# Kernel tuning notes

Measured on AMD Instinct MI355X. Metric: run time of the kernel, lower is better.

## Reference

```python
import jax, jax.numpy as jnp
import numpy as np

B, S, H = 8, 32, 2048          # batch, block (query) length, hidden size
NH, NKV, HD = 16, 2, 128       # attention heads, kv heads, head_dim
KV_LEN = 8192                  # block kv-cache length
GROUPS = NH // NKV
SCALE = HD ** -0.5


def rotate_half(x):
    x1, x2 = jnp.split(x, 2, axis=-1)
    return jnp.concatenate((-x2, x1), axis=-1)


def setup_inputs() -> dict:
    key = jax.random.key(0)
    ks = jax.random.split(key, 12)
    inv_freq = 1.0 / (10000.0 ** (jnp.arange(0, HD, 2, dtype=jnp.float32) / HD))
    pos = jnp.arange(S, dtype=jnp.float32)[:, None] * inv_freq[None, :]  # [S, HD/2]
    ang = jnp.concatenate([pos, pos], axis=-1)                           # [S, HD]
    cos = jnp.broadcast_to(jnp.cos(ang)[None], (B, S, HD))
    sin = jnp.broadcast_to(jnp.sin(ang)[None], (B, S, HD))
    s = 0.02
    return {
        'hidden_states': jax.random.normal(ks[0], (B, S, H), jnp.float32),
        'cos': cos,
        'sin': sin,
        'k_cache': jax.random.normal(ks[1], (B, NKV, KV_LEN, HD), jnp.float32),
        'v_cache': jax.random.normal(ks[2], (B, NKV, KV_LEN, HD), jnp.float32),
        'attention_mask': jnp.zeros((B, 1, S, KV_LEN), jnp.float32),
        'replace_position': 4096,
        'q_w': jax.random.normal(ks[3], (H, NH * HD), jnp.float32) * s,
        'q_b': jax.random.normal(ks[4], (NH * HD,), jnp.float32) * s,
        'k_w': jax.random.normal(ks[5], (H, NKV * HD), jnp.float32) * s,
        'k_b': jax.random.normal(ks[6], (NKV * HD,), jnp.float32) * s,
        'v_w': jax.random.normal(ks[7], (H, NKV * HD), jnp.float32) * s,
        'v_b': jax.random.normal(ks[8], (NKV * HD,), jnp.float32) * s,
        'o_w': jax.random.normal(ks[9], (NH * HD, H), jnp.float32) * s,
    }


def reference(hidden_states, cos, sin, k_cache, v_cache, attention_mask,
              replace_position, q_w, q_b, k_w, k_b, v_w, v_b, o_w):
    # fused QKV projections -> [B, heads, S, HD]
    q = (hidden_states @ q_w + q_b).reshape(B, S, NH, HD).transpose(0, 2, 1, 3)
    k = (hidden_states @ k_w + k_b).reshape(B, S, NKV, HD).transpose(0, 2, 1, 3)
    v = (hidden_states @ v_w + v_b).reshape(B, S, NKV, HD).transpose(0, 2, 1, 3)

    # RoPE (cos/sin unsqueezed on the head dim)
    c = cos[:, None]  # [B,1,S,HD]
    s_ = sin[:, None]
    q = q * c + rotate_half(q) * s_
    k = k * c + rotate_half(k) * s_

    # block KV-cache in-place update at replace_position
    k_all = jax.lax.dynamic_update_slice(k_cache, k, (0, 0, replace_position, 0))
    v_all = jax.lax.dynamic_update_slice(v_cache, v, (0, 0, replace_position, 0))

    # GQA: expand kv heads to match attention heads
    k_all = jnp.repeat(k_all, GROUPS, axis=1)  # [B,NH,KV,HD]
    v_all = jnp.repeat(v_all, GROUPS, axis=1)

    # SDPA with additive mask (is_causal=False)
    scores = jnp.einsum('bhqd,bhkd->bhqk', q, k_all) * SCALE + attention_mask
    probs = jax.nn.softmax(scores, axis=-1)
    attn = jnp.einsum('bhqk,bhkd->bhqd', probs, v_all)  # [B,NH,S,HD]

    out = attn.transpose(0, 2, 1, 3).reshape(B, S, NH * HD)
    return out @ o_w
```

## Files before the change

### kernel.cpp

```cpp
#include <hip/hip_runtime.h>
#include <hip/hip_bf16.h>

#define B_    8
#define S_    32
#define H_    2048
#define NH_   16
#define NKV_  2
#define HD_   128
#define KV_   8192
#define G_    8
#define M_    256
#define NQKV  2560
#define NSP   16
#define KT_   64
#define NT_   8
#define SCALE_ 0.08838834764831845f
#define CFIX_  8.0f

typedef __bf16 bf16x8 __attribute__((ext_vector_type(8)));
typedef float  f32x4  __attribute__((ext_vector_type(4)));
typedef float  f32x16 __attribute__((ext_vector_type(16)));

__device__ __forceinline__ unsigned short f2b(float f){
  unsigned u = __float_as_uint(f);
  u = u + 0x7FFFu + ((u>>16)&1u);
  return (unsigned short)(u>>16);
}
__device__ __forceinline__ float b2f(unsigned short h){
  return __uint_as_float(((unsigned)h)<<16);
}
__device__ __forceinline__ unsigned pk2(float a, float b){
  return (unsigned)f2b(a) | ((unsigned)f2b(b)<<16);
}
__device__ __forceinline__ unsigned cvtpk(float lo, float hi){
  unsigned r;
  asm("v_cvt_pk_bf16_f32 %0, %1, %2" : "=v"(r) : "v"(lo), "v"(hi));
  return r;
}
__device__ __forceinline__ bf16x8 ld_frag(const unsigned short* p){
  union { uint4 u; bf16x8 b; } cv;
  cv.u = *(const uint4*)p;
  return cv.b;
}
__device__ __forceinline__ f32x4 mf(bf16x8 a, bf16x8 b, f32x4 c){
  return __builtin_amdgcn_mfma_f32_16x16x32_bf16(a, b, c, 0, 0, 0);
}
__device__ __forceinline__ f32x16 mf32(bf16x8 a, bf16x8 b, f32x16 c){
  return __builtin_amdgcn_mfma_f32_32x32x16_bf16(a, b, c, 0, 0, 0);
}
__device__ __forceinline__ int swiK(int row, int col){
  return row*128 + (col ^ ((((row)&15) ^ ((row>>1)&8)) << 3));
}
__device__ __forceinline__ int swiV(int row, int col){
  return row*64 + (col ^ (((row)&7) << 3));
}

__global__ __launch_bounds__(256) void k_cvt(const float* __restrict__ x,
                                             unsigned short* __restrict__ y){
  const int i = (blockIdx.x*256 + threadIdx.x)*4;
  const float4 v = *(const float4*)(x + i);
  ushort4 o; o.x=f2b(v.x); o.y=f2b(v.y); o.z=f2b(v.z); o.w=f2b(v.w);
  *(ushort4*)(y + i) = o;
}

__global__ __launch_bounds__(256) void k_gemm_qkv(
    const unsigned short* __restrict__ A,
    const float* __restrict__ qw, const float* __restrict__ kw, const float* __restrict__ vw,
    const float* __restrict__ qbv, const float* __restrict__ kbv, const float* __restrict__ vbv,
    float* __restrict__ rawp)
{
  __shared__ unsigned short As[64][56];
  __shared__ unsigned short Bs[64][56];
  const int n0 = blockIdx.x*64, m0 = blockIdx.y*64, kz = blockIdx.z;
  const float* W; const float* bias; int ldw, wc0;
  if(n0 < 2048)      { W=qw; bias=qbv; ldw=2048; wc0=n0; }
  else if(n0 < 2304) { W=kw; bias=kbv; ldw=256;  wc0=n0-2048; }
  else               { W=vw; bias=vbv; ldw=256;  wc0=n0-2304; }
  const int t = threadIdx.x, lane = t&63, wid = t>>6;
  const int wr = wid>>1, wc = wid&1, l15 = lane&15, lq = lane>>4;
  const int ar = t>>2,  ac = (t&3)*8;
  const int bk = t>>5,  bn = (t&31)*2;
  f32x4 acc[2][2] = {};
  for(int k0 = kz*1024; k0 < kz*1024 + 1024; k0 += 32){
    __syncthreads();
    *(uint4*)(&As[ar][ac]) = *(const uint4*)(A + (m0+ar)*2048 + k0 + ac);
    #pragma unroll
    for(int p=0;p<4;p++){
      const int kk = bk + p*8;
      const float2 wv = *(const float2*)(W + (long)(k0+kk)*ldw + wc0 + bn);
      Bs[bn  ][kk] = f2b(wv.x);
      Bs[bn+1][kk] = f2b(wv.y);
    }
    __syncthreads();
    const bf16x8 a0 = ld_frag(&As[wr*32      + l15][lq*8]);
    const bf16x8 a1 = ld_frag(&As[wr*32 + 16 + l15][lq*8]);
    const bf16x8 b0 = ld_frag(&Bs[wc*32      + l15][lq*8]);
    const bf16x8 b1 = ld_frag(&Bs[wc*32 + 16 + l15][lq*8]);
    acc[0][0] = mf(a0,b0,acc[0][0]);
    acc[0][1] = mf(a0,b1,acc[0][1]);
    acc[1][0] = mf(a1,b0,acc[1][0]);
    acc[1][1] = mf(a1,b1,acc[1][1]);
  }
  float* out = rawp + (long)kz*M_*NQKV;
  #pragma unroll
  for(int mi=0;mi<2;mi++)
    #pragma unroll
    for(int nj=0;nj<2;nj++){
      const int col = n0 + wc*32 + nj*16 + l15;
      const float bv = kz ? 0.f : bias[wc0 + wc*32 + nj*16 + l15];
      #pragma unroll
      for(int rr=0;rr<4;rr++){
        const int row = m0 + wr*32 + mi*16 + lq*4 + rr;
        out[row*NQKV + col] = acc[mi][nj][rr] + bv;
      }
    }
}

__global__ __launch_bounds__(128) void k_rope(
    const float* __restrict__ rawp, const float* __restrict__ cosb, const float* __restrict__ sinb,
    unsigned short* __restrict__ Qb, float* __restrict__ KnF, float* __restrict__ VnF)
{
  const int r = blockIdx.x, hh = blockIdx.y, d = threadIdx.x;
  const int b = r>>5, s = r&31;
  const float cv = cosb[(b*S_+s)*HD_ + d];
  const float sv = sinb[(b*S_+s)*HD_ + d];
  const int dp = (d<64)? d+64 : d-64;
  #define RAW2(c) (rawp[r*NQKV + (c)] + rawp[(long)M_*NQKV + r*NQKV + (c)])
  if(hh < 16){
    const float x  = RAW2(hh*HD_ + d);
    const float xo = RAW2(hh*HD_ + dp);
    const float y  = x*cv + ((d<64)? -xo : xo)*sv;
    const int kvh = hh>>3, g = hh&7;
    Qb[((long)(b*NKV_+kvh)*M_ + g*S_ + s)*HD_ + d] = f2b(y);
  } else if(hh < 18){
    const int kvh = hh-16;
    const float x  = RAW2(2048 + kvh*HD_ + d);
    const float xo = RAW2(2048 + kvh*HD_ + dp);
    KnF[((long)(b*NKV_+kvh)*S_ + s)*HD_ + d] = x*cv + ((d<64)? -xo : xo)*sv;
  } else {
    const int kvh = hh-18;
    VnF[((long)(b*NKV_+kvh)*S_ + s)*HD_ + d] = RAW2(2304 + kvh*HD_ + d);
  }
  #undef RAW2
}

__global__ __launch_bounds__(256) void k_mswz(const float* __restrict__ mask,
                                              float* __restrict__ msw){
  const int g = blockIdx.x*256 + threadIdx.x;
  const int b = g >> 16, q = (g>>11)&31, c4 = g & 2047;
  const int kv = c4*4;
  const int sp = kv>>9, tt = (kv>>6)&7, kvt = (kv>>5)&1, r4 = (kv>>3)&3, hi = (kv>>2)&1;
  const int lane = q + 32*hi;
  float4 v = *(const float4*)(mask + ((long)b*S_ + q)*KV_ + kv);
  v.x -= CFIX_; v.y -= CFIX_; v.z -= CFIX_; v.w -= CFIX_;
  const long dst = ((((long)(b*NSP+sp)*NT_ + tt)*64 + lane)*8 + kvt*4 + r4);
  *(float4*)(msw + dst*4) = v;
}

__global__ __launch_bounds__(512, 2) void k_attn(
    const unsigned short* __restrict__ Qb,
    const float* __restrict__ KnF, const float* __restrict__ VnF,
    const float* __restrict__ kc, const float* __restrict__ vc,
    const float* __restrict__ msw, const int* __restrict__ rpp,
    unsigned short* __restrict__ num, float* __restrict__ mbuf, float* __restrict__ lbuf)
{
  __shared__ __align__(16) unsigned short lds[2][2][KT_*128];
  const int sp = blockIdx.x, kvh = blockIdx.y, b = blockIdx.z;
  const int bk = b*NKV_ + kvh;
  const int rp = *rpp;
  const int t = threadIdx.x, lane = t&63, wid = t>>6;
  const int l31 = lane&31, hi = lane>>5;
  const int kvbase = sp*(KV_/NSP);
  const int krow = t>>3, kc0 = (t&7)*16;
  const int vhd  = t&127, vkq = t>>7;
  const int cbsK = (hi*8) ^ ((((l31)&15) ^ ((l31>>1)&8)) << 3);
  const int cbsV = (hi*8) ^ (((l31)&7) << 3);
  const int rowK = l31*128, rowV = l31*64;
  const int wk0 = swiK(krow, kc0), wk1 = swiK(krow, kc0+8);
  const int wv0 = swiV(vhd, vkq*16), wv1 = swiV(vhd, vkq*16+8);

  bf16x8 qf[8];
  { const unsigned short* qp = Qb + ((long)bk*M_ + wid*32 + l31)*HD_;
    #pragma unroll
    for(int ks=0;ks<8;ks++) qf[ks] = ld_frag(qp + ks*16 + hi*8); }

  float4 vK4[4];
  float  vV[16];
  float4 vM[8];
  const float4* mbase = (const float4*)msw + ((long)(b*NSP+sp)*NT_)*64*8 + lane*8;

  auto loadK = [&](int tt){
    const int kvr = kvbase + tt*KT_ + krow;
    const float* kp = (kvr>=rp && kvr<rp+S_)
        ? (KnF + ((long)bk*S_ + (kvr-rp))*HD_ + kc0)
        : (kc  + ((long)bk*KV_ + kvr)*HD_ + kc0);
    #pragma unroll
    for(int i=0;i<4;i++) vK4[i] = *(const float4*)(kp + i*4);
  };
  auto loadV = [&](int tt){
    #pragma unroll
    for(int m=0;m<16;m++){
      const int kvr = kvbase + tt*KT_ + vkq*16 + m;
      const float* vp = (kvr>=rp && kvr<rp+S_)
          ? (VnF + ((long)bk*S_ + (kvr-rp))*HD_)
          : (vc  + ((long)bk*KV_ + kvr)*HD_);
      vV[m] = vp[vhd];
    }
  };
  auto loadM = [&](int tt){
    const float4* mp = mbase + (long)tt*64*8;
    #pragma unroll
    for(int j=0;j<8;j++) vM[j] = mp[j];
  };
  auto writeK = [&](int bb){
    unsigned short* Sb = &lds[bb][0][0];
    uint4 w4;
    w4.x = cvtpk(vK4[0].x, vK4[0].y);  w4.y = cvtpk(vK4[0].z, vK4[0].w);
    w4.z = cvtpk(vK4[1].x, vK4[1].y);  w4.w = cvtpk(vK4[1].z, vK4[1].w);
    *(uint4*)(Sb + wk0) = w4;
    w4.x = cvtpk(vK4[2].x, vK4[2].y);  w4.y = cvtpk(vK4[2].z, vK4[2].w);
    w4.z = cvtpk(vK4[3].x, vK4[3].y);  w4.w = cvtpk(vK4[3].z, vK4[3].w);
    *(uint4*)(Sb + wk1) = w4;
  };
  auto writeV = [&](int bb){
    unsigned short* Sb = &lds[bb][1][0];
    uint4 w4;
    w4.x = cvtpk(vV[0], vV[1]);   w4.y = cvtpk(vV[2], vV[3]);
    w4.z = cvtpk(vV[4], vV[5]);   w4.w = cvtpk(vV[6], vV[7]);
    *(uint4*)(Sb + wv0) = w4;
    w4.x = cvtpk(vV[8], vV[9]);   w4.y = cvtpk(vV[10], vV[11]);
    w4.z = cvtpk(vV[12], vV[13]); w4.w = cvtpk(vV[14], vV[15]);
    *(uint4*)(Sb + wv1) = w4;
  };

  loadK(0); loadV(0);
  writeK(0); writeV(0);
  __syncthreads();

  f32x16 oc[4] = {};
  float l_run = 0.f;

  for(int tt=0; tt<NT_; tt++){
    const int cur = tt&1;
    loadM(tt);
    if(tt<NT_-1){ loadK(tt+1); loadV(tt+1); }
    f32x16 sc[2] = {};
    { const unsigned short* Sk = &lds[cur][0][0];
      __builtin_amdgcn_s_setprio(1);
      #pragma unroll
      for(int ks=0;ks<8;ks++){
        #pragma unroll
        for(int kvt=0;kvt<2;kvt++)
          sc[kvt] = mf32(ld_frag(Sk + rowK + kvt*4096 + (cbsK ^ (ks*16))), qf[ks], sc[kvt]);
      }
      __builtin_amdgcn_s_setprio(0);
    }
    float psum = 0.f;
    #pragma unroll
    for(int kvt=0;kvt<2;kvt++){
      #pragma unroll
      for(int r4=0;r4<4;r4++){
        const float4 mk = vM[kvt*4+r4];
        const float p0 = __expf(fmaf(sc[kvt][r4*4+0], SCALE_, mk.x));
        const float p1 = __expf(fmaf(sc[kvt][r4*4+1], SCALE_, mk.y));
        const float p2 = __expf(fmaf(sc[kvt][r4*4+2], SCALE_, mk.z));
        const float p3 = __expf(fmaf(sc[kvt][r4*4+3], SCALE_, mk.w));
        sc[kvt][r4*4+0]=p0; sc[kvt][r4*4+1]=p1;
        sc[kvt][r4*4+2]=p2; sc[kvt][r4*4+3]=p3;
        psum += (p0+p1)+(p2+p3);
      }
    }
    l_run += psum;
    unsigned w_[2][4][2];
    #pragma unroll
    for(int kvt=0;kvt<2;kvt++)
      #pragma unroll
      for(int r4=0;r4<4;r4++){
        w_[kvt][r4][0] = cvtpk(sc[kvt][r4*4+0], sc[kvt][r4*4+1]);
        w_[kvt][r4][1] = cvtpk(sc[kvt][r4*4+2], sc[kvt][r4*4+3]);
      }
    { const unsigned short* Sv = &lds[cur][1][0];
      __builtin_amdgcn_s_setprio(1);
      #pragma unroll
      for(int kvs=0;kvs<4;kvs++){
        const int kvt = kvs>>1, k2 = (kvs&1)*2;
        const unsigned wa0 = w_[kvt][k2  ][0], wa1 = w_[kvt][k2  ][1];
        const unsigned wb0 = w_[kvt][k2+1][0], wb1 = w_[kvt][k2+1][1];
        const unsigned own0 = hi? wb0:wa0, own1 = hi? wb1:wa1;
        const unsigned snd0 = hi? wa0:wb0, snd1 = hi? wa1:wb1;
        const unsigned rcv0 = __shfl_xor(snd0, 32, 64);
        const unsigned rcv1 = __shfl_xor(snd1, 32, 64);
        union{ unsigned u[4]; bf16x8 v; } ap;
        ap.u[0] = hi? rcv0:own0;  ap.u[1] = hi? rcv1:own1;
        ap.u[2] = hi? own0:rcv0;  ap.u[3] = hi? own1:rcv1;
        #pragma unroll
        for(int ht=0;ht<4;ht++)
          oc[ht] = mf32(ap.v, ld_frag(Sv + rowV + ht*2048 + (cbsV ^ (kvs*16))), oc[ht]);
      }
      __builtin_amdgcn_s_setprio(0);
    }
    if(tt<NT_-1){ writeK(cur^1); writeV(cur^1); }
    __syncthreads();
  }

  const float l_tot = l_run + __shfl_xor(l_run, 32, 64);
  if(lane < 32){
    const long base = ((long)bk*NSP + sp)*M_ + wid*32 + lane;
    mbuf[base] = CFIX_;
    lbuf[base] = l_tot;
  }
  unsigned short* np_ = num + (((long)bk*NSP + sp)*M_ + wid*32)*HD_;
  #pragma unroll
  for(int ht=0;ht<4;ht++)
    #pragma unroll
    for(int r4=0;r4<4;r4++)
      #pragma unroll
      for(int rr=0;rr<4;rr++){
        const int q = rr + 8*r4 + 4*hi;
        np_[(long)q*HD_ + ht*32 + l31] = f2b(oc[ht][r4*4+rr]);
      }
}

__global__ __launch_bounds__(128) void k_comb(
    const unsigned short* __restrict__ num, const float* __restrict__ mbuf,
    const float* __restrict__ lbuf, unsigned short* __restrict__ attnb)
{
  const int q = blockIdx.x, kvh = blockIdx.y, b = blockIdx.z, d = threadIdx.x;
  const int bk = b*NKV_ + kvh;
  float M = -3.0e38f;
  #pragma unroll
  for(int c=0;c<NSP;c++) M = fmaxf(M, mbuf[((long)bk*NSP + c)*M_ + q]);
  float den = 0.f, acc = 0.f;
  #pragma unroll
  for(int c=0;c<NSP;c++){
    const long ix = ((long)bk*NSP + c)*M_ + q;
    const float w = __expf(mbuf[ix] - M);
    den += lbuf[ix]*w;
    acc += w * b2f(num[ix*HD_ + d]);
  }
  const int g = q>>5, s = q&31, h = kvh*G_ + g;
  attnb[((long)(b*S_+s))*2048 + h*HD_ + d] = f2b(acc/den);
}

__global__ __launch_bounds__(256) void k_gemm_o(
    const unsigned short* __restrict__ A,
    const float* __restrict__ W,
    float* __restrict__ owsp)
{
  __shared__ unsigned short As[64][56];
  __shared__ unsigned short Bs[64][56];
  const int n0 = blockIdx.x*64, m0 = blockIdx.y*64, kz = blockIdx.z;
  const int t = threadIdx.x, lane = t&63, wid = t>>6;
  const int wr = wid>>1, wc = wid&1, l15 = lane&15, lq = lane>>4;
  const int ar = t>>2,  ac = (t&3)*8;
  const int bk = t>>5,  bn = (t&31)*2;
  f32x4 acc[2][2] = {};
  for(int k0 = kz*1024; k0 < kz*1024 + 1024; k0 += 32){
    __syncthreads();
    *(uint4*)(&As[ar][ac]) = *(const uint4*)(A + (m0+ar)*2048 + k0 + ac);
    #pragma unroll
    for(int p=0;p<4;p++){
      const int kk = bk + p*8;
      const float2 wv = *(const float2*)(W + (long)(k0+kk)*2048 + n0 + bn);
      Bs[bn  ][kk] = f2b(wv.x);
      Bs[bn+1][kk] = f2b(wv.y);
    }
    __syncthreads();
    const bf16x8 a0 = ld_frag(&As[wr*32      + l15][lq*8]);
    const bf16x8 a1 = ld_frag(&As[wr*32 + 16 + l15][lq*8]);
    const bf16x8 b0 = ld_frag(&Bs[wc*32      + l15][lq*8]);
    const bf16x8 b1 = ld_frag(&Bs[wc*32 + 16 + l15][lq*8]);
    acc[0][0] = mf(a0,b0,acc[0][0]);
    acc[0][1] = mf(a0,b1,acc[0][1]);
    acc[1][0] = mf(a1,b0,acc[1][0]);
    acc[1][1] = mf(a1,b1,acc[1][1]);
  }
  float* out = owsp + (long)kz*M_*2048;
  #pragma unroll
  for(int mi=0;mi<2;mi++)
    #pragma unroll
    for(int nj=0;nj<2;nj++){
      const int col = n0 + wc*32 + nj*16 + l15;
      #pragma unroll
      for(int rr=0;rr<4;rr++){
        const int row = m0 + wr*32 + mi*16 + lq*4 + rr;
        out[row*2048 + col] = acc[mi][nj][rr];
      }
    }
}

__global__ __launch_bounds__(256) void k_ored(const float* __restrict__ a,
                                              float* __restrict__ out){
  const int i = (blockIdx.x*256 + threadIdx.x)*4;
  const float4 x = *(const float4*)(a + i);
  const float4 y = *(const float4*)(a + (long)M_*2048 + i);
  float4 o; o.x=x.x+y.x; o.y=x.y+y.y; o.z=x.z+y.z; o.w=x.w+y.w;
  *(float4*)(out + i) = o;
}

extern "C" void kernel_launch(void* const* d_in, const int* in_sizes, int n_in,
                              void* d_out, int out_size, void* d_ws, size_t ws_size,
                              hipStream_t stream){
  (void)in_sizes; (void)n_in; (void)out_size; (void)ws_size;
  const float* hs   = (const float*)d_in[0];
  const float* cosb = (const float*)d_in[1];
  const float* sinb = (const float*)d_in[2];
  const float* kc   = (const float*)d_in[3];
  const float* vc   = (const float*)d_in[4];
  const float* mask = (const float*)d_in[5];
  const int*   rp   = (const int*)  d_in[6];
  const float* qw   = (const float*)d_in[7];
  const float* qb   = (const float*)d_in[8];
  const float* kw   = (const float*)d_in[9];
  const float* kb   = (const float*)d_in[10];
  const float* vw   = (const float*)d_in[11];
  const float* vb   = (const float*)d_in[12];
  const float* ow   = (const float*)d_in[13];
  char* ws = (char*)d_ws;
  unsigned short* hsb   = (unsigned short*)(ws + 0);
  float*          rawp  = (float*)         (ws + 1048576);
  unsigned short* Qb    = (unsigned short*)(ws + 6291456);
  float*          KnF   = (float*)         (ws + 7340032);
  float*          VnF   = (float*)         (ws + 7602176);
  unsigned short* attnb = (unsigned short*)(ws + 7864320);
  float*          mbuf  = (float*)         (ws + 8912896);
  float*          lbuf  = (float*)         (ws + 9175040);
  unsigned short* num   = (unsigned short*)(ws + 9437184);
  float*          owsp  = (float*)         (ws + 26214400);
  float*          msw   = (float*)         (ws + 30408704);
  float* outp = (float*)d_out;

  k_cvt     <<<dim3(512),        dim3(256),  0, stream>>>(hs, hsb);
  k_gemm_qkv<<<dim3(40,4,2),     dim3(256),  0, stream>>>(hsb, qw,kw,vw, qb,kb,vb, rawp);
  k_mswz    <<<dim3(2048),       dim3(256),  0, stream>>>(mask, msw);
  k_rope    <<<dim3(256,20),     dim3(128),  0, stream>>>(rawp, cosb, sinb, Qb, KnF, VnF);
  k_attn    <<<dim3(NSP,2,8),    dim3(512),  0, stream>>>(Qb, KnF, VnF, kc, vc, msw, rp, num, mbuf, lbuf);
  k_comb    <<<dim3(256,2,8),    dim3(128),  0, stream>>>(num, mbuf, lbuf, attnb);
  k_gemm_o  <<<dim3(32,4,2),     dim3(256),  0, stream>>>(attnb, ow, owsp);
  k_ored    <<<dim3(512),        dim3(256),  0, stream>>>(owsp, outp);
}
```

Before: 122.6 us.

## Fuse input cast into QKV GEMM, raise split-K, deepen attention pipeline, use exp2

Measured after the change: 107.8 us. 12.1% less time.

```diff
diff --git a/kernel.cpp b/kernel.cpp
--- a/kernel.cpp
+++ b/kernel.cpp
@@ -16,6 +16,8 @@
 #define NT_   8
 #define SCALE_ 0.08838834764831845f
 #define CFIX_  8.0f
+#define LOG2E_ 1.4426950408889634f
+#define SCALE2_ (SCALE_*LOG2E_)
 
 typedef __bf16 bf16x8 __attribute__((ext_vector_type(8)));
 typedef float  f32x4  __attribute__((ext_vector_type(4)));
@@ -29,14 +31,18 @@
 __device__ __forceinline__ float b2f(unsigned short h){
   return __uint_as_float(((unsigned)h)<<16);
 }
-__device__ __forceinline__ unsigned pk2(float a, float b){
-  return (unsigned)f2b(a) | ((unsigned)f2b(b)<<16);
-}
 __device__ __forceinline__ unsigned cvtpk(float lo, float hi){
   unsigned r;
   asm("v_cvt_pk_bf16_f32 %0, %1, %2" : "=v"(r) : "v"(lo), "v"(hi));
   return r;
 }
+__device__ __forceinline__ float fexp2(float x){
+#if __has_builtin(__builtin_amdgcn_exp2f)
+  return __builtin_amdgcn_exp2f(x);
+#else
+  return __expf(x * 0.6931471805599453f);
+#endif
+}
 __device__ __forceinline__ bf16x8 ld_frag(const unsigned short* p){
   union { uint4 u; bf16x8 b; } cv;
   cv.u = *(const uint4*)p;
@@ -55,16 +61,8 @@
   return row*64 + (col ^ (((row)&7) << 3));
 }
 
-__global__ __launch_bounds__(256) void k_cvt(const float* __restrict__ x,
-                                             unsigned short* __restrict__ y){
-  const int i = (blockIdx.x*256 + threadIdx.x)*4;
-  const float4 v = *(const float4*)(x + i);
-  ushort4 o; o.x=f2b(v.x); o.y=f2b(v.y); o.z=f2b(v.z); o.w=f2b(v.w);
-  *(ushort4*)(y + i) = o;
-}
-
 __global__ __launch_bounds__(256) void k_gemm_qkv(
-    const unsigned short* __restrict__ A,
+    const float* __restrict__ A,
     const float* __restrict__ qw, const float* __restrict__ kw, const float* __restrict__ vw,
     const float* __restrict__ qbv, const float* __restrict__ kbv, const float* __restrict__ vbv,
     float* __restrict__ rawp)
@@ -81,9 +79,13 @@
   const int ar = t>>2,  ac = (t&3)*8;
   const int bk = t>>5,  bn = (t&31)*2;
   f32x4 acc[2][2] = {};
-  for(int k0 = kz*1024; k0 < kz*1024 + 1024; k0 += 32){
+  for(int k0 = kz*512; k0 < kz*512 + 512; k0 += 32){
     __syncthreads();
-    *(uint4*)(&As[ar][ac]) = *(const uint4*)(A + (m0+ar)*2048 + k0 + ac);
+    { const float4 a0 = *(const float4*)(A + (m0+ar)*2048 + k0 + ac);
+      const float4 a1 = *(const float4*)(A + (m0+ar)*2048 + k0 + ac + 4);
+      uint4 w4; w4.x=cvtpk(a0.x,a0.y); w4.y=cvtpk(a0.z,a0.w);
+                w4.z=cvtpk(a1.x,a1.y); w4.w=cvtpk(a1.z,a1.w);
+      *(uint4*)(&As[ar][ac]) = w4; }
     #pragma unroll
     for(int p=0;p<4;p++){
       const int kk = bk + p*8;
@@ -122,26 +124,27 @@
 {
   const int r = blockIdx.x, hh = blockIdx.y, d = threadIdx.x;
   const int b = r>>5, s = r&31;
+  const long MN = (long)M_*NQKV;
   const float cv = cosb[(b*S_+s)*HD_ + d];
   const float sv = sinb[(b*S_+s)*HD_ + d];
   const int dp = (d<64)? d+64 : d-64;
-  #define RAW2(c) (rawp[r*NQKV + (c)] + rawp[(long)M_*NQKV + r*NQKV + (c)])
+  #define RAW4(c) (rawp[r*NQKV+(c)] + rawp[MN+r*NQKV+(c)] + rawp[2*MN+r*NQKV+(c)] + rawp[3*MN+r*NQKV+(c)])
   if(hh < 16){
-    const float x  = RAW2(hh*HD_ + d);
-    const float xo = RAW2(hh*HD_ + dp);
+    const float x  = RAW4(hh*HD_ + d);
+    const float xo = RAW4(hh*HD_ + dp);
     const float y  = x*cv + ((d<64)? -xo : xo)*sv;
     const int kvh = hh>>3, g = hh&7;
     Qb[((long)(b*NKV_+kvh)*M_ + g*S_ + s)*HD_ + d] = f2b(y);
   } else if(hh < 18){
     const int kvh = hh-16;
-    const float x  = RAW2(2048 + kvh*HD_ + d);
-    const float xo = RAW2(2048 + kvh*HD_ + dp);
+    const float x  = RAW4(2048 + kvh*HD_ + d);
+    const float xo = RAW4(2048 + kvh*HD_ + dp);
     KnF[((long)(b*NKV_+kvh)*S_ + s)*HD_ + d] = x*cv + ((d<64)? -xo : xo)*sv;
   } else {
     const int kvh = hh-18;
-    VnF[((long)(b*NKV_+kvh)*S_ + s)*HD_ + d] = RAW2(2304 + kvh*HD_ + d);
-  }
-  #undef RAW2
+    VnF[((long)(b*NKV_+kvh)*S_ + s)*HD_ + d] = RAW4(2304 + kvh*HD_ + d);
+  }
+  #undef RAW4
 }
 
 __global__ __launch_bounds__(256) void k_mswz(const float* __restrict__ mask,
@@ -152,7 +155,8 @@
   const int sp = kv>>9, tt = (kv>>6)&7, kvt = (kv>>5)&1, r4 = (kv>>3)&3, hi = (kv>>2)&1;
   const int lane = q + 32*hi;
   float4 v = *(const float4*)(mask + ((long)b*S_ + q)*KV_ + kv);
-  v.x -= CFIX_; v.y -= CFIX_; v.z -= CFIX_; v.w -= CFIX_;
+  v.x = (v.x - CFIX_)*LOG2E_; v.y = (v.y - CFIX_)*LOG2E_;
+  v.z = (v.z - CFIX_)*LOG2E_; v.w = (v.w - CFIX_)*LOG2E_;
   const long dst = ((((long)(b*NSP+sp)*NT_ + tt)*64 + lane)*8 + kvt*4 + r4);
   *(float4*)(msw + dst*4) = v;
 }
@@ -164,7 +168,7 @@
     const float* __restrict__ msw, const int* __restrict__ rpp,
     unsigned short* __restrict__ num, float* __restrict__ mbuf, float* __restrict__ lbuf)
 {
-  __shared__ __align__(16) unsigned short lds[2][2][KT_*128];
+  __shared__ __align__(16) unsigned short lds[4][2][KT_*128];
   const int sp = blockIdx.x, kvh = blockIdx.y, b = blockIdx.z;
   const int bk = b*NKV_ + kvh;
   const int rp = *rpp;
@@ -186,7 +190,6 @@
 
   float4 vK4[4];
   float  vV[16];
-  float4 vM[8];
   const float4* mbase = (const float4*)msw + ((long)(b*NSP+sp)*NT_)*64*8 + lane*8;
 
   auto loadK = [&](int tt){
@@ -206,11 +209,6 @@
           : (vc  + ((long)bk*KV_ + kvr)*HD_);
       vV[m] = vp[vhd];
     }
-  };
-  auto loadM = [&](int tt){
-    const float4* mp = mbase + (long)tt*64*8;
-    #pragma unroll
-    for(int j=0;j<8;j++) vM[j] = mp[j];
   };
   auto writeK = [&](int bb){
     unsigned short* Sb = &lds[bb][0][0];
@@ -233,19 +231,16 @@
     *(uint4*)(Sb + wv1) = w4;
   };
 
-  loadK(0); loadV(0);
-  writeK(0); writeV(0);
-  __syncthreads();
-
   f32x16 oc[4] = {};
   float l_run = 0.f;
 
-  for(int tt=0; tt<NT_; tt++){
-    const int cur = tt&1;
-    loadM(tt);
-    if(tt<NT_-1){ loadK(tt+1); loadV(tt+1); }
+  auto process = [&](int buf, int tt){
+    float4 vM[8];
+    { const float4* mp = mbase + (long)tt*64*8;
+      #pragma unroll
+      for(int j=0;j<8;j++) vM[j] = mp[j]; }
     f32x16 sc[2] = {};
-    { const unsigned short* Sk = &lds[cur][0][0];
+    { const unsigned short* Sk = &lds[buf][0][0];
       __builtin_amdgcn_s_setprio(1);
       #pragma unroll
       for(int ks=0;ks<8;ks++){
@@ -261,10 +256,10 @@
       #pragma unroll
       for(int r4=0;r4<4;r4++){
         const float4 mk = vM[kvt*4+r4];
-        const float p0 = __expf(fmaf(sc[kvt][r4*4+0], SCALE_, mk.x));
-        const float p1 = __expf(fmaf(sc[kvt][r4*4+1], SCALE_, mk.y));
-        const float p2 = __expf(fmaf(sc[kvt][r4*4+2], SCALE_, mk.z));
-        const float p3 = __expf(fmaf(sc[kvt][r4*4+3], SCALE_, mk.w));
+        const float p0 = fexp2(fmaf(sc[kvt][r4*4+0], SCALE2_, mk.x));
+        const float p1 = fexp2(fmaf(sc[kvt][r4*4+1], SCALE2_, mk.y));
+        const float p2 = fexp2(fmaf(sc[kvt][r4*4+2], SCALE2_, mk.z));
+        const float p3 = fexp2(fmaf(sc[kvt][r4*4+3], SCALE2_, mk.w));
         sc[kvt][r4*4+0]=p0; sc[kvt][r4*4+1]=p1;
         sc[kvt][r4*4+2]=p2; sc[kvt][r4*4+3]=p3;
         psum += (p0+p1)+(p2+p3);
@@ -279,7 +274,7 @@
         w_[kvt][r4][0] = cvtpk(sc[kvt][r4*4+0], sc[kvt][r4*4+1]);
         w_[kvt][r4][1] = cvtpk(sc[kvt][r4*4+2], sc[kvt][r4*4+3]);
       }
-    { const unsigned short* Sv = &lds[cur][1][0];
+    { const unsigned short* Sv = &lds[buf][1][0];
       __builtin_amdgcn_s_setprio(1);
       #pragma unroll
       for(int kvs=0;kvs<4;kvs++){
@@ -299,7 +294,22 @@
       }
       __builtin_amdgcn_s_setprio(0);
     }
-    if(tt<NT_-1){ writeK(cur^1); writeV(cur^1); }
+  };
+
+  loadK(0); loadV(0); writeK(0); writeV(0);
+  loadK(1); loadV(1); writeK(1); writeV(1);
+  __syncthreads();
+
+  for(int it=0; it<4; ++it){
+    const int tA = 2*it, tB = tA+1;
+    const int bA = (it&1)*2, bB = bA+1;
+    const int wA = bA^2,     wB = bB^2;
+    if(tA+2 < NT_){ loadK(tA+2); loadV(tA+2); }
+    process(bA, tA);
+    if(tA+2 < NT_){ writeK(wA); writeV(wA); }
+    if(tB+2 < NT_){ loadK(tB+2); loadV(tB+2); }
+    process(bB, tB);
+    if(tB+2 < NT_){ writeK(wB); writeV(wB); }
     __syncthreads();
   }
 
@@ -355,7 +365,7 @@
   const int ar = t>>2,  ac = (t&3)*8;
   const int bk = t>>5,  bn = (t&31)*2;
   f32x4 acc[2][2] = {};
-  for(int k0 = kz*1024; k0 < kz*1024 + 1024; k0 += 32){
+  for(int k0 = kz*512; k0 < kz*512 + 512; k0 += 32){
     __syncthreads();
     *(uint4*)(&As[ar][ac]) = *(const uint4*)(A + (m0+ar)*2048 + k0 + ac);
     #pragma unroll
@@ -392,9 +402,13 @@
 __global__ __launch_bounds__(256) void k_ored(const float* __restrict__ a,
                                               float* __restrict__ out){
   const int i = (blockIdx.x*256 + threadIdx.x)*4;
+  const long MN = (long)M_*2048;
   const float4 x = *(const float4*)(a + i);
-  const float4 y = *(const float4*)(a + (long)M_*2048 + i);
-  float4 o; o.x=x.x+y.x; o.y=x.y+y.y; o.z=x.z+y.z; o.w=x.w+y.w;
+  const float4 y = *(const float4*)(a + MN + i);
+  const float4 z = *(const float4*)(a + 2*MN + i);
+  const float4 w = *(const float4*)(a + 3*MN + i);
+  float4 o; o.x=(x.x+y.x)+(z.x+w.x); o.y=(x.y+y.y)+(z.y+w.y);
+            o.z=(x.z+y.z)+(z.z+w.z); o.w=(x.w+y.w)+(z.w+w.w);
   *(float4*)(out + i) = o;
 }
 
@@ -417,25 +431,23 @@
   const float* vb   = (const float*)d_in[12];
   const float* ow   = (const float*)d_in[13];
   char* ws = (char*)d_ws;
-  unsigned short* hsb   = (unsigned short*)(ws + 0);
-  float*          rawp  = (float*)         (ws + 1048576);
-  unsigned short* Qb    = (unsigned short*)(ws + 6291456);
-  float*          KnF   = (float*)         (ws + 7340032);
-  float*          VnF   = (float*)         (ws + 7602176);
-  unsigned short* attnb = (unsigned short*)(ws + 7864320);
-  float*          mbuf  = (float*)         (ws + 8912896);
-  float*          lbuf  = (float*)         (ws + 9175040);
-  unsigned short* num   = (unsigned short*)(ws + 9437184);
-  float*          owsp  = (float*)         (ws + 26214400);
-  float*          msw   = (float*)         (ws + 30408704);
+  float*          rawp  = (float*)         (ws + 0);
+  unsigned short* Qb    = (unsigned short*)(ws + 10485760);
+  float*          KnF   = (float*)         (ws + 11534336);
+  float*          VnF   = (float*)         (ws + 11796480);
+  unsigned short* attnb = (unsigned short*)(ws + 12058624);
+  float*          mbuf  = (float*)         (ws + 13107200);
+  float*          lbuf  = (float*)         (ws + 13369344);
+  unsigned short* num   = (unsigned short*)(ws + 13631488);
+  float*          owsp  = (float*)         (ws + 30408704);
+  float*          msw   = (float*)         (ws + 38797312);
   float* outp = (float*)d_out;
 
-  k_cvt     <<<dim3(512),        dim3(256),  0, stream>>>(hs, hsb);
-  k_gemm_qkv<<<dim3(40,4,2),     dim3(256),  0, stream>>>(hsb, qw,kw,vw, qb,kb,vb, rawp);
+  k_gemm_qkv<<<dim3(40,4,4),     dim3(256),  0, stream>>>(hs, qw,kw,vw, qb,kb,vb, rawp);
   k_mswz    <<<dim3(2048),       dim3(256),  0, stream>>>(mask, msw);
   k_rope    <<<dim3(256,20),     dim3(128),  0, stream>>>(rawp, cosb, sinb, Qb, KnF, VnF);
   k_attn    <<<dim3(NSP,2,8),    dim3(512),  0, stream>>>(Qb, KnF, VnF, kc, vc, msw, rp, num, mbuf, lbuf);
   k_comb    <<<dim3(256,2,8),    dim3(128),  0, stream>>>(num, mbuf, lbuf, attnb);
-  k_gemm_o  <<<dim3(32,4,2),     dim3(256),  0, stream>>>(attnb, ow, owsp);
+  k_gemm_o  <<<dim3(32,4,4),     dim3(256),  0, stream>>>(attnb, ow, owsp);
   k_ored    <<<dim3(512),        dim3(256),  0, stream>>>(owsp, outp);
 }
```
